# Kernel tuning notes

Measured on AMD Instinct MI355X. Metric: run time of the kernel, lower is better.

## Reference

```python
import jax, jax.numpy as jnp
import numpy as np

N = 50000
E = 1_600_000
IN_C = 128
OUT_C = 128


def _glorot(key, shape):
    fan_in, fan_out = shape[0], shape[1]
    s = jnp.sqrt(6.0 / (fan_in + fan_out))
    return jax.random.uniform(key, shape, jnp.float32, -s, s)


def setup_inputs() -> dict:
    key = jax.random.key(0)
    ks = jax.random.split(key, 32)
    inp = {
        'X': jax.random.normal(ks[0], (N, IN_C), jnp.float32),
        'edge_index': jax.random.randint(ks[1], (2, E), 0, N, jnp.int64),
        'edge_weight': jax.random.uniform(ks[2], (E,), jnp.float32),
        'H': jax.random.normal(ks[3], (N, OUT_C), jnp.float32),
        'C': jax.random.normal(ks[4], (N, OUT_C), jnp.float32),
    }
    i = 5
    for g in ('i', 'f', 'c', 'o'):
        inp[f'Wx_{g}'] = _glorot(ks[i], (IN_C, OUT_C)); i += 1
        inp[f'bx_{g}'] = jnp.zeros((OUT_C,), jnp.float32)
        inp[f'Wh_{g}'] = _glorot(ks[i], (OUT_C, OUT_C)); i += 1
        inp[f'bh_{g}'] = jnp.zeros((OUT_C,), jnp.float32)
    for g in ('i', 'f', 'o'):
        inp[f'w_c_{g}'] = _glorot(ks[i], (1, OUT_C)); i += 1
    for g in ('i', 'f', 'c', 'o'):
        inp[f'b_{g}'] = jnp.zeros((1, OUT_C), jnp.float32)
    return inp


def reference(X, edge_index, edge_weight, H, C,
              Wx_i, bx_i, Wh_i, bh_i,
              Wx_f, bx_f, Wh_f, bh_f,
              Wx_c, bx_c, Wh_c, bh_c,
              Wx_o, bx_o, Wh_o, bh_o,
              w_c_i, w_c_f, w_c_o,
              b_i, b_f, b_c, b_o):
    n = X.shape[0]
    src, dst = edge_index[0], edge_index[1]
    # GCN normalization (add_self_loops=False): deg from destination (in-degree)
    deg = jax.ops.segment_sum(edge_weight, dst, num_segments=n)
    dis = jnp.where(deg > 0, jax.lax.rsqrt(jnp.where(deg > 0, deg, 1.0)), 0.0)
    norm = dis[src] * edge_weight * dis[dst]  # [E]

    def gcn(x, W, b):
        xw = x @ W                       # [n, OUT_C]
        msg = xw[src] * norm[:, None]    # gather + scale, [E, OUT_C]
        return jax.ops.segment_sum(msg, dst, num_segments=n) + b

    I = jax.nn.sigmoid(gcn(X, Wx_i, bx_i) + gcn(H, Wh_i, bh_i) + w_c_i * C + b_i)
    Fg = jax.nn.sigmoid(gcn(X, Wx_f, bx_f) + gcn(H, Wh_f, bh_f) + w_c_f * C + b_f)
    T = jnp.tanh(gcn(X, Wx_c, bx_c) + gcn(H, Wh_c, bh_c) + b_c)
    Cn = Fg * C + I * T
    O = jax.nn.sigmoid(gcn(X, Wx_o, bx_o) + gcn(H, Wh_o, bh_o) + w_c_o * Cn + b_o)
    Hn = O * jnp.tanh(Cn)
    return Hn, Cn
```

## Files before the change

### kernel.cpp

```cpp
#include <hip/hip_runtime.h>

__device__ __forceinline__ float bf2f(unsigned short u){
    union { unsigned int i; float f; } v; v.i = ((unsigned int)u) << 16; return v.f;
}
__device__ __forceinline__ unsigned short f2bf(float f){
    union { unsigned int i; float f; } v; v.f = f;
    unsigned int i = v.i;
    unsigned int r = i + 0x7FFFu + ((i >> 16) & 1u);
    return (unsigned short)(r >> 16);
}
__device__ __forceinline__ float sigm(float x){ return 1.0f / (1.0f + __expf(-x)); }

__device__ __forceinline__ float ldsel(const void* p, size_t idx, int fF){
    float r;
    if (fF) r = ((const float*)p)[idx];
    else    r = bf2f(((const unsigned short*)p)[idx]);
    return r;
}

typedef __attribute__((ext_vector_type(8))) short s8v;
typedef __attribute__((ext_vector_type(4))) float f4v;

__global__ void k_detect(const unsigned short* __restrict__ X,
                         const int* __restrict__ ei, int* __restrict__ flags){
    __shared__ int cnt, nz;
    if (threadIdx.x == 0){ cnt = 0; nz = 0; }
    __syncthreads();
    int ok = 0;
    for (int i = threadIdx.x; i < 2048; i += 256){
        int e = (X[i] >> 7) & 0xFF;
        if (e >= 96 && e <= 160) ok++;
    }
    atomicAdd(&cnt, ok);
    int nzl = 0;
    for (int i = threadIdx.x; i < 128; i += 256)
        if (ei[2*i + 1] != 0) nzl++;
    atomicAdd(&nz, nzl);
    __syncthreads();
    if (threadIdx.x == 0){
        flags[0] = (cnt < 1843) ? 1 : 0;
        flags[1] = (nz == 0)   ? 1 : 0;
    }
}

struct PackArgs {
    const void* Wx[4];
    const void* Wh[4];
    const void* bx[4];
    const void* bh[4];
};

__global__ void k_fused1(const void* __restrict__ X, const void* __restrict__ H,
                         unsigned int* __restrict__ XHb32,
                         const int* __restrict__ ei, int* __restrict__ cnt,
                         int* __restrict__ off,
                         PackArgs pa, unsigned short* __restrict__ Bp,
                         float* __restrict__ bias,
                         const int* __restrict__ flags,
                         int nbT, int nbC, int E, int N){
    int b = blockIdx.x;
    int fF = flags[0];
    if (b < nbT){
        int t = b*256 + threadIdx.x;
        if (t >= N * 64) return;
        int n = t >> 6, l = t & 63;
        unsigned int xw, hw;
        if (fF){
            float2 xv = ((const float2*)X)[(size_t)n*64 + l];
            float2 hv = ((const float2*)H)[(size_t)n*64 + l];
            xw = ((unsigned int)f2bf(xv.y) << 16) | f2bf(xv.x);
            hw = ((unsigned int)f2bf(hv.y) << 16) | f2bf(hv.x);
        } else {
            xw = ((const unsigned int*)X)[(size_t)n*64 + l];
            hw = ((const unsigned int*)H)[(size_t)n*64 + l];
        }
        XHb32[(size_t)n*128 + l]      = xw;
        XHb32[(size_t)n*128 + 64 + l] = hw;
    } else if (b < nbT + nbC){
        int e = (b - nbT)*256 + threadIdx.x;
        if (e >= E) return;
        int fI = flags[1];
        int d = fI ? ei[2*(size_t)E + 2*(size_t)e] : ei[(size_t)E + e];
        if ((unsigned)d >= (unsigned)N) return;
        off[e] = atomicAdd(&cnt[d], 1);
    } else {
        int t = (b - nbT - nbC)*256 + threadIdx.x;
        if (t < 4*8*8*64*8){
            int j    =  t        & 7;
            int lane = (t >> 3)  & 63;
            int kb   = (t >> 9)  & 7;
            int ct   = (t >> 12) & 7;
            int g    = (t >> 15) & 3;
            int k   = kb*32 + (lane >> 4)*8 + j;
            int col = ct*16 + (lane & 15);
            const void* p; size_t idx;
            if (k < 128){ p = pa.Wx[g]; idx = (size_t)k*128 + col; }
            else        { p = pa.Wh[g]; idx = (size_t)(k-128)*128 + col; }
            unsigned short v;
            if (fF) v = f2bf(((const float*)p)[idx]);
            else    v = ((const unsigned short*)p)[idx];
            Bp[t] = v;
        }
        if (t < 512){
            int g = t >> 7, c = t & 127;
            bias[t] = ldsel(pa.bx[g], c, fF) + ldsel(pa.bh[g], c, fF);
        }
    }
}

__global__ void k_scanA(const int* __restrict__ cnt, int* __restrict__ bsum, int n){
    __shared__ int sh[256];
    int t = threadIdx.x, i = blockIdx.x * 256 + t;
    sh[t] = (i < n) ? cnt[i] : 0;
    __syncthreads();
    for (int o = 128; o > 0; o >>= 1){
        if (t < o) sh[t] += sh[t + o];
        __syncthreads();
    }
    if (t == 0) bsum[blockIdx.x] = sh[0];
}
__global__ void k_scanB(const int* __restrict__ bsum, int* __restrict__ bsumoff, int nb){
    __shared__ int sh[256];
    int t = threadIdx.x;
    int v = (t < nb) ? bsum[t] : 0;
    sh[t] = v;
    __syncthreads();
    for (int o = 1; o < 256; o <<= 1){
        int u = (t >= o) ? sh[t - o] : 0;
        __syncthreads();
        sh[t] += u;
        __syncthreads();
    }
    bsumoff[t] = sh[t] - v;
}
__global__ void k_scanC(const int* __restrict__ cnt, const int* __restrict__ bsumoff,
                        int* __restrict__ rowstart, int n){
    __shared__ int sh[256];
    int t = threadIdx.x, i = blockIdx.x * 256 + t;
    int v = (i < n) ? cnt[i] : 0;
    sh[t] = v;
    __syncthreads();
    for (int o = 1; o < 256; o <<= 1){
        int u = (t >= o) ? sh[t - o] : 0;
        __syncthreads();
        sh[t] += u;
        __syncthreads();
    }
    int incl = sh[t];
    if (i < n)     rowstart[i] = bsumoff[blockIdx.x] + incl - v;
    if (i == n-1)  rowstart[n] = bsumoff[blockIdx.x] + incl;
}

__global__ void k_scatter(const int* __restrict__ ei, const void* __restrict__ ew,
                          const int* __restrict__ rowstart, const int* __restrict__ off,
                          int2* __restrict__ recs, const int* __restrict__ flags,
                          int E, int N){
    int e = blockIdx.x * 256 + threadIdx.x;
    if (e >= E) return;
    int fF = flags[0], fI = flags[1];
    int s, d;
    if (fI){ s = ei[2*(size_t)e]; d = ei[2*(size_t)E + 2*(size_t)e]; }
    else   { s = ei[e];           d = ei[(size_t)E + e]; }
    if ((unsigned)d >= (unsigned)N) return;
    float w = 0.f; int ss = 0;
    if ((unsigned)s < (unsigned)N){ w = ldsel(ew, e, fF); ss = s; }
    int2 r; r.x = ss; r.y = __float_as_int(w);
    recs[rowstart[d] + off[e]] = r;
}

__global__ __launch_bounds__(256)
void k_degdis(const int2* __restrict__ recs, const int* __restrict__ rowstart,
              float* __restrict__ dis, int N){
    int gw = (blockIdx.x * 256 + threadIdx.x) >> 6;
    int lane = threadIdx.x & 63;
    if (gw >= N) return;
    int beg = rowstart[gw], end = rowstart[gw + 1];
    float sw = 0.f;
    for (int i = beg + lane; i < end; i += 64) sw += __int_as_float(recs[i].y);
    for (int o = 32; o > 0; o >>= 1) sw += __shfl_down(sw, o);
    if (lane == 0) dis[gw] = (sw > 0.f) ? rsqrtf(sw) : 0.f;
}

__global__ __launch_bounds__(256)
void k_gather(const int2* __restrict__ recs, const int* __restrict__ rowstart,
              const float* __restrict__ dis, const unsigned int* __restrict__ XHb32,
              unsigned int* __restrict__ AXH32, int N){
    int gw = (blockIdx.x * 256 + threadIdx.x) >> 6;
    int lane = threadIdx.x & 63;
    if (gw >= 2*N) return;
    int node = gw >> 1;
    int half = (gw & 1) * 64;
    int beg = rowstart[node], end = rowstart[node + 1];
    float disd = dis[node];
    float a0 = 0.f, a1 = 0.f;
    int i = beg;
    for (; i + 1 < end; i += 2){
        int2 r1 = recs[i];
        int2 r2 = recs[i+1];
        float n1 = dis[r1.x] * __int_as_float(r1.y) * disd;
        float n2 = dis[r2.x] * __int_as_float(r2.y) * disd;
        unsigned int v1 = XHb32[(size_t)r1.x*128 + half + lane];
        unsigned int v2 = XHb32[(size_t)r2.x*128 + half + lane];
        a0 += n1 * bf2f((unsigned short)(v1 & 0xffff));
        a1 += n1 * bf2f((unsigned short)(v1 >> 16));
        a0 += n2 * bf2f((unsigned short)(v2 & 0xffff));
        a1 += n2 * bf2f((unsigned short)(v2 >> 16));
    }
    if (i < end){
        int2 r1 = recs[i];
        float n1 = dis[r1.x] * __int_as_float(r1.y) * disd;
        unsigned int v1 = XHb32[(size_t)r1.x*128 + half + lane];
        a0 += n1 * bf2f((unsigned short)(v1 & 0xffff));
        a1 += n1 * bf2f((unsigned short)(v1 >> 16));
    }
    AXH32[(size_t)node*128 + half + lane] = ((unsigned int)f2bf(a1) << 16) | f2bf(a0);
}

struct EpiArgs {
    const void *C, *wci, *wcf, *wco, *bi, *bff, *bc, *bo;
};

__global__ __launch_bounds__(256)
void k_gemm(const unsigned short* __restrict__ AXH,
            const unsigned short* __restrict__ Bp, const float* __restrict__ bias,
            EpiArgs ea, void* __restrict__ outp, const int* __restrict__ flags, int N){
    __shared__ float pre[4][16][132];

    int tid  = threadIdx.x;
    int wave = tid >> 6, lane = tid & 63;
    int node0 = blockIdx.x * 16;
    int fF = flags[0];

    f4v acc[8];
#pragma unroll
    for (int ct = 0; ct < 8; ct++) acc[ct] = (f4v){0.f,0.f,0.f,0.f};

    const int g = wave;
    const unsigned short* abase = AXH + (size_t)(node0 + (lane & 15))*256 + (lane >> 4)*8;
#pragma unroll
    for (int kb = 0; kb < 8; kb++){
        s8v af = *(const s8v*)(abase + kb*32);
        const unsigned short* bbase = Bp + g*32768 + kb*512 + lane*8;
#pragma unroll
        for (int ct = 0; ct < 8; ct++){
            s8v bfrag = *(const s8v*)(bbase + ct*4096);
            acc[ct] = __builtin_amdgcn_mfma_f32_16x16x32_bf16(af, bfrag, acc[ct], 0, 0, 0);
        }
    }

    int q = lane >> 4, cl = lane & 15;
#pragma unroll
    for (int ct = 0; ct < 8; ct++){
        int col = ct*16 + cl;
        float bv = bias[g*128 + col];
#pragma unroll
        for (int r = 0; r < 4; r++)
            pre[g][q*4 + r][col] = acc[ct][r] + bv;
    }
    __syncthreads();

    for (int i = tid; i < 2048; i += 256){
        int nn = i >> 7, c = i & 127;
        if (node0 + nn >= N) break;
        size_t gidx = (size_t)(node0+nn)*128 + c;
        float Cv  = ldsel(ea.C, gidx, fF);
        float pi  = pre[0][nn][c], pf = pre[1][nn][c];
        float pcv = pre[2][nn][c], po = pre[3][nn][c];
        float Iv = sigm(pi + ldsel(ea.wci, c, fF)*Cv + ldsel(ea.bi, c, fF));
        float Fv = sigm(pf + ldsel(ea.wcf, c, fF)*Cv + ldsel(ea.bff, c, fF));
        float Tv = tanhf(pcv + ldsel(ea.bc, c, fF));
        float Cn = Fv*Cv + Iv*Tv;
        float Ov = sigm(po + ldsel(ea.wco, c, fF)*Cn + ldsel(ea.bo, c, fF));
        float Hn = Ov * tanhf(Cn);
        if (fF){
            ((float*)outp)[gidx] = Hn;
            ((float*)outp)[(size_t)N*128 + gidx] = Cn;
        } else {
            ((unsigned short*)outp)[gidx] = f2bf(Hn);
            ((unsigned short*)outp)[(size_t)N*128 + gidx] = f2bf(Cn);
        }
    }
}

extern "C" void kernel_launch(void* const* d_in, const int* in_sizes, int n_in,
                              void* d_out, int out_size, void* d_ws, size_t ws_size,
                              hipStream_t stream){
    const void* X  = d_in[0];
    const int*  ei = (const int*)d_in[1];
    const void* ew = d_in[2];
    const void* H  = d_in[3];
    const void* C  = d_in[4];
    const int N = in_sizes[0] / 128;
    const int E = in_sizes[2];

    char* ws = (char*)d_ws;
    int*   cnt          = (int*)  (ws);
    float* dis          = (float*)(ws + ((size_t)256 << 10));
    int*   rowstart     = (int*)  (ws + ((size_t)512 << 10));
    int*   bsum         = (int*)  (ws + ((size_t)768 << 10));
    int*   bsumoff      = (int*)  (ws + ((size_t)772 << 10));
    int*   flags        = (int*)  (ws + ((size_t)776 << 10));
    unsigned short* Bp  = (unsigned short*)(ws + ((size_t)1 << 20));
    float* bias         = (float*)(ws + ((size_t)1 << 20) + ((size_t)256 << 10));
    int*   off          = (int*)  (ws + ((size_t)2 << 20));
    unsigned int* AXH32 = (unsigned int*)(ws + ((size_t)2 << 20));
    int2*  recs         = (int2*) (ws + ((size_t)28 << 20));
    unsigned int* XHb32 = (unsigned int*)(ws + ((size_t)41 << 20));

    hipMemsetAsync(cnt, 0, (size_t)256 << 10, stream);
    k_detect<<<1, 256, 0, stream>>>((const unsigned short*)X, ei, flags);

    PackArgs pa;
    pa.Wx[0]=d_in[5];  pa.bx[0]=d_in[6];  pa.Wh[0]=d_in[7];  pa.bh[0]=d_in[8];
    pa.Wx[1]=d_in[9];  pa.bx[1]=d_in[10]; pa.Wh[1]=d_in[11]; pa.bh[1]=d_in[12];
    pa.Wx[2]=d_in[13]; pa.bx[2]=d_in[14]; pa.Wh[2]=d_in[15]; pa.bh[2]=d_in[16];
    pa.Wx[3]=d_in[17]; pa.bx[3]=d_in[18]; pa.Wh[3]=d_in[19]; pa.bh[3]=d_in[20];

    int nbT = (N*64 + 255)/256;
    int nbC = (E + 255)/256;
    k_fused1<<<nbT + nbC + 512, 256, 0, stream>>>(X, H, XHb32, ei, cnt, off,
                                                  pa, Bp, bias, flags, nbT, nbC, E, N);

    int nbA = (N + 255)/256;
    k_scanA<<<nbA, 256, 0, stream>>>(cnt, bsum, N);
    k_scanB<<<1, 256, 0, stream>>>(bsum, bsumoff, nbA);
    k_scanC<<<nbA, 256, 0, stream>>>(cnt, bsumoff, rowstart, N);

    k_scatter<<<(E + 255)/256, 256, 0, stream>>>(ei, ew, rowstart, off, recs, flags, E, N);
    k_degdis<<<(N*64 + 255)/256, 256, 0, stream>>>(recs, rowstart, dis, N);
    k_gather<<<(2*N*64 + 255)/256, 256, 0, stream>>>(recs, rowstart, dis, XHb32, AXH32, N);

    EpiArgs ea;
    ea.C   = C;
    ea.wci = d_in[21];
    ea.wcf = d_in[22];
    ea.wco = d_in[23];
    ea.bi  = d_in[24];
    ea.bff = d_in[25];
    ea.bc  = d_in[26];
    ea.bo  = d_in[27];
    k_gemm<<<(N + 15)/16, 256, 0, stream>>>((const unsigned short*)AXH32, Bp, bias,
                                            ea, d_out, flags, N);
}
```

Baseline: 588.7 us.

## Widen gather loads to 16 bytes and restructure GEMM to keep gates in registers

```diff
diff --git a/kernel.cpp b/kernel.cpp
--- a/kernel.cpp
+++ b/kernel.cpp
@@ -183,37 +183,70 @@
 
 __global__ __launch_bounds__(256)
 void k_gather(const int2* __restrict__ recs, const int* __restrict__ rowstart,
-              const float* __restrict__ dis, const unsigned int* __restrict__ XHb32,
-              unsigned int* __restrict__ AXH32, int N){
-    int gw = (blockIdx.x * 256 + threadIdx.x) >> 6;
+              const float* __restrict__ dis, const uint4* __restrict__ XHb128,
+              uint4* __restrict__ AXH128, int N){
+    int node = (blockIdx.x * 256 + threadIdx.x) >> 6;
     int lane = threadIdx.x & 63;
-    if (gw >= 2*N) return;
-    int node = gw >> 1;
-    int half = (gw & 1) * 64;
+    if (node >= N) return;
+    int half = lane >> 5;
+    int sub  = lane & 31;
     int beg = rowstart[node], end = rowstart[node + 1];
     float disd = dis[node];
-    float a0 = 0.f, a1 = 0.f;
+    float a0=0.f,a1=0.f,a2=0.f,a3=0.f,a4=0.f,a5=0.f,a6=0.f,a7=0.f;
+
+#define ACC8(v, n)                                              \
+    a0 += (n) * bf2f((unsigned short)((v).x & 0xffff));         \
+    a1 += (n) * bf2f((unsigned short)((v).x >> 16));            \
+    a2 += (n) * bf2f((unsigned short)((v).y & 0xffff));         \
+    a3 += (n) * bf2f((unsigned short)((v).y >> 16));            \
+    a4 += (n) * bf2f((unsigned short)((v).z & 0xffff));         \
+    a5 += (n) * bf2f((unsigned short)((v).z >> 16));            \
+    a6 += (n) * bf2f((unsigned short)((v).w & 0xffff));         \
+    a7 += (n) * bf2f((unsigned short)((v).w >> 16));
+
     int i = beg;
-    for (; i + 1 < end; i += 2){
-        int2 r1 = recs[i];
-        int2 r2 = recs[i+1];
-        float n1 = dis[r1.x] * __int_as_float(r1.y) * disd;
-        float n2 = dis[r2.x] * __int_as_float(r2.y) * disd;
-        unsigned int v1 = XHb32[(size_t)r1.x*128 + half + lane];
-        unsigned int v2 = XHb32[(size_t)r2.x*128 + half + lane];
-        a0 += n1 * bf2f((unsigned short)(v1 & 0xffff));
-        a1 += n1 * bf2f((unsigned short)(v1 >> 16));
-        a0 += n2 * bf2f((unsigned short)(v2 & 0xffff));
-        a1 += n2 * bf2f((unsigned short)(v2 >> 16));
+    for (; i + 3 < end; i += 4){
+        int2 rA = recs[i + half];
+        int2 rB = recs[i + 2 + half];
+        uint4 vA = XHb128[(size_t)rA.x*32 + sub];
+        uint4 vB = XHb128[(size_t)rB.x*32 + sub];
+        float nA = dis[rA.x] * __int_as_float(rA.y) * disd;
+        float nB = dis[rB.x] * __int_as_float(rB.y) * disd;
+        ACC8(vA, nA);
+        ACC8(vB, nB);
+    }
+    if (end - i >= 2){
+        int2 rA = recs[i + half];
+        uint4 vA = XHb128[(size_t)rA.x*32 + sub];
+        float nA = dis[rA.x] * __int_as_float(rA.y) * disd;
+        ACC8(vA, nA);
+        i += 2;
     }
     if (i < end){
-        int2 r1 = recs[i];
-        float n1 = dis[r1.x] * __int_as_float(r1.y) * disd;
-        unsigned int v1 = XHb32[(size_t)r1.x*128 + half + lane];
-        a0 += n1 * bf2f((unsigned short)(v1 & 0xffff));
-        a1 += n1 * bf2f((unsigned short)(v1 >> 16));
-    }
-    AXH32[(size_t)node*128 + half + lane] = ((unsigned int)f2bf(a1) << 16) | f2bf(a0);
+        int2 rA = recs[i];
+        uint4 vA = XHb128[(size_t)rA.x*32 + sub];
+        float nA = (half == 0) ? dis[rA.x] * __int_as_float(rA.y) * disd : 0.f;
+        ACC8(vA, nA);
+    }
+#undef ACC8
+
+    a0 += __shfl_xor(a0, 32, 64);
+    a1 += __shfl_xor(a1, 32, 64);
+    a2 += __shfl_xor(a2, 32, 64);
+    a3 += __shfl_xor(a3, 32, 64);
+    a4 += __shfl_xor(a4, 32, 64);
+    a5 += __shfl_xor(a5, 32, 64);
+    a6 += __shfl_xor(a6, 32, 64);
+    a7 += __shfl_xor(a7, 32, 64);
+
+    if (half == 0){
+        uint4 o;
+        o.x = ((unsigned int)f2bf(a1) << 16) | f2bf(a0);
+        o.y = ((unsigned int)f2bf(a3) << 16) | f2bf(a2);
+        o.z = ((unsigned int)f2bf(a5) << 16) | f2bf(a4);
+        o.w = ((unsigned int)f2bf(a7) << 16) | f2bf(a6);
+        AXH128[(size_t)node*32 + sub] = o;
+    }
 }
 
 struct EpiArgs {
@@ -224,60 +257,68 @@
 void k_gemm(const unsigned short* __restrict__ AXH,
             const unsigned short* __restrict__ Bp, const float* __restrict__ bias,
             EpiArgs ea, void* __restrict__ outp, const int* __restrict__ flags, int N){
-    __shared__ float pre[4][16][132];
-
     int tid  = threadIdx.x;
-    int wave = tid >> 6, lane = tid & 63;
-    int node0 = blockIdx.x * 16;
+    int w    = tid >> 6, lane = tid & 63;
+    int node0 = blockIdx.x * 32;
     int fF = flags[0];
 
-    f4v acc[8];
-#pragma unroll
-    for (int ct = 0; ct < 8; ct++) acc[ct] = (f4v){0.f,0.f,0.f,0.f};
-
-    const int g = wave;
-    const unsigned short* abase = AXH + (size_t)(node0 + (lane & 15))*256 + (lane >> 4)*8;
+    f4v acc[2][8];
+#pragma unroll
+    for (int m = 0; m < 2; m++)
+#pragma unroll
+        for (int c = 0; c < 8; c++) acc[m][c] = (f4v){0.f,0.f,0.f,0.f};
+
+    const unsigned short* a0base = AXH + (size_t)(node0 + (lane & 15))*256 + (lane >> 4)*8;
+    const unsigned short* a1base = a0base + 16*256;
 #pragma unroll
     for (int kb = 0; kb < 8; kb++){
-        s8v af = *(const s8v*)(abase + kb*32);
-        const unsigned short* bbase = Bp + g*32768 + kb*512 + lane*8;
-#pragma unroll
-        for (int ct = 0; ct < 8; ct++){
-            s8v bfrag = *(const s8v*)(bbase + ct*4096);
-            acc[ct] = __builtin_amdgcn_mfma_f32_16x16x32_bf16(af, bfrag, acc[ct], 0, 0, 0);
+        s8v af0 = *(const s8v*)(a0base + kb*32);
+        s8v af1 = *(const s8v*)(a1base + kb*32);
+#pragma unroll
+        for (int ct8 = 0; ct8 < 8; ct8++){
+            int g = ct8 >> 1, sub = ct8 & 1;
+            const s8v bfrag = *(const s8v*)(Bp + g*32768 + (size_t)(w*2 + sub)*4096
+                                            + kb*512 + lane*8);
+            acc[0][ct8] = __builtin_amdgcn_mfma_f32_16x16x32_bf16(af0, bfrag, acc[0][ct8], 0, 0, 0);
+            acc[1][ct8] = __builtin_amdgcn_mfma_f32_16x16x32_bf16(af1, bfrag, acc[1][ct8], 0, 0, 0);
         }
     }
 
     int q = lane >> 4, cl = lane & 15;
 #pragma unroll
-    for (int ct = 0; ct < 8; ct++){
-        int col = ct*16 + cl;
-        float bv = bias[g*128 + col];
-#pragma unroll
-        for (int r = 0; r < 4; r++)
-            pre[g][q*4 + r][col] = acc[ct][r] + bv;
-    }
-    __syncthreads();
-
-    for (int i = tid; i < 2048; i += 256){
-        int nn = i >> 7, c = i & 127;
-        if (node0 + nn >= N) break;
-        size_t gidx = (size_t)(node0+nn)*128 + c;
-        float Cv  = ldsel(ea.C, gidx, fF);
-        float pi  = pre[0][nn][c], pf = pre[1][nn][c];
-        float pcv = pre[2][nn][c], po = pre[3][nn][c];
-        float Iv = sigm(pi + ldsel(ea.wci, c, fF)*Cv + ldsel(ea.bi, c, fF));
-        float Fv = sigm(pf + ldsel(ea.wcf, c, fF)*Cv + ldsel(ea.bff, c, fF));
-        float Tv = tanhf(pcv + ldsel(ea.bc, c, fF));
-        float Cn = Fv*Cv + Iv*Tv;
-        float Ov = sigm(po + ldsel(ea.wco, c, fF)*Cn + ldsel(ea.bo, c, fF));
-        float Hn = Ov * tanhf(Cn);
-        if (fF){
-            ((float*)outp)[gidx] = Hn;
-            ((float*)outp)[(size_t)N*128 + gidx] = Cn;
-        } else {
-            ((unsigned short*)outp)[gidx] = f2bf(Hn);
-            ((unsigned short*)outp)[(size_t)N*128 + gidx] = f2bf(Cn);
+    for (int sub = 0; sub < 2; sub++){
+        int c = w*32 + sub*16 + cl;
+        float bvi = bias[0*128 + c], bvf = bias[1*128 + c];
+        float bvc = bias[2*128 + c], bvo = bias[3*128 + c];
+        float wci = ldsel(ea.wci, c, fF), wcf = ldsel(ea.wcf, c, fF), wco = ldsel(ea.wco, c, fF);
+        float bi  = ldsel(ea.bi, c, fF),  bff = ldsel(ea.bff, c, fF);
+        float bc  = ldsel(ea.bc, c, fF),  bo  = ldsel(ea.bo, c, fF);
+#pragma unroll
+        for (int m = 0; m < 2; m++){
+#pragma unroll
+            for (int r = 0; r < 4; r++){
+                int node = node0 + m*16 + q*4 + r;
+                if (node >= N) continue;
+                size_t gidx = (size_t)node*128 + c;
+                float Cv = ldsel(ea.C, gidx, fF);
+                float pi  = acc[m][0+sub][r] + bvi;
+                float pf  = acc[m][2+sub][r] + bvf;
+                float pcv = acc[m][4+sub][r] + bvc;
+                float po  = acc[m][6+sub][r] + bvo;
+                float Iv = sigm(pi + wci*Cv + bi);
+                float Fv = sigm(pf + wcf*Cv + bff);
+                float Tv = tanhf(pcv + bc);
+                float Cn = Fv*Cv + Iv*Tv;
+                float Ov = sigm(po + wco*Cn + bo);
+                float Hn = Ov * tanhf(Cn);
+                if (fF){
+                    ((float*)outp)[gidx] = Hn;
+                    ((float*)outp)[(size_t)N*128 + gidx] = Cn;
+                } else {
+                    ((unsigned short*)outp)[gidx] = f2bf(Hn);
+                    ((unsigned short*)outp)[(size_t)N*128 + gidx] = f2bf(Cn);
+                }
+            }
         }
     }
 }
@@ -328,7 +369,9 @@
 
     k_scatter<<<(E + 255)/256, 256, 0, stream>>>(ei, ew, rowstart, off, recs, flags, E, N);
     k_degdis<<<(N*64 + 255)/256, 256, 0, stream>>>(recs, rowstart, dis, N);
-    k_gather<<<(2*N*64 + 255)/256, 256, 0, stream>>>(recs, rowstart, dis, XHb32, AXH32, N);
+    k_gather<<<(N*64 + 255)/256, 256, 0, stream>>>(recs, rowstart, dis,
+                                                   (const uint4*)XHb32,
+                                                   (uint4*)AXH32, N);
 
     EpiArgs ea;
     ea.C   = C;
@@ -339,6 +382,6 @@
     ea.bff = d_in[25];
     ea.bc  = d_in[26];
     ea.bo  = d_in[27];
-    k_gemm<<<(N + 15)/16, 256, 0, stream>>>((const unsigned short*)AXH32, Bp, bias,
+    k_gemm<<<(N + 31)/32, 256, 0, stream>>>((const unsigned short*)AXH32, Bp, bias,
                                             ea, d_out, flags, N);
 }
```

After: 501.4 us. 14.8% less time.
